# Kernel optimization log

Measured on AMD Instinct MI355X. Metric: run time of the kernel, lower is better.

Reference implementation:

```python
import jax, jax.numpy as jnp
import numpy as np
from jax import lax

KS = 3
N = KS * KS  # 9 sampling locations per output pixel


def conv2d(x, w, b, pad, dil=1):
    out = lax.conv_general_dilated(
        x, w, window_strides=(1, 1), padding=((pad, pad), (pad, pad)),
        rhs_dilation=(dil, dil), dimension_numbers=('NCHW', 'OIHW', 'NCHW'))
    return out + b[None, :, None, None]


def deform_conv(x, p_w, p_b, dw, db):
    # Pure deform-conv-v2 semantics: offsets from p_conv, bilinear gather on
    # zero-padded input, then 3x3 contraction over the 9 gathered samples.
    B, C, H, W = x.shape
    offset = conv2d(x, p_w, p_b, 1)                       # (B, 2N, H, W)
    xp = jnp.pad(x, ((0, 0), (0, 0), (1, 1), (1, 1)))     # zero pad by 1
    Hp, Wp = H + 2, W + 2
    rr = jnp.arange(-(KS // 2), KS // 2 + 1)
    pi, pj = jnp.meshgrid(rr, rr, indexing='ij')
    p_n = jnp.concatenate([pi.reshape(-1), pj.reshape(-1)]).astype(x.dtype)   # (2N,)
    gi, gj = jnp.meshgrid(jnp.arange(1, H + 1), jnp.arange(1, W + 1), indexing='ij')
    p0 = jnp.concatenate([jnp.broadcast_to(gi, (N, H, W)),
                          jnp.broadcast_to(gj, (N, H, W))], 0).astype(x.dtype)  # (2N,H,W)
    p = p0[None] + p_n[None, :, None, None] + offset      # (B, 2N, H, W)
    p = jnp.transpose(p, (0, 2, 3, 1))                    # (B, H, W, 2N)
    py, px = p[..., :N], p[..., N:]
    fy, fx = jnp.floor(py), jnp.floor(px)
    lt_y = jnp.clip(fy, 0, Hp - 1); lt_x = jnp.clip(fx, 0, Wp - 1)
    rb_y = jnp.clip(fy + 1, 0, Hp - 1); rb_x = jnp.clip(fx + 1, 0, Wp - 1)
    pyc = jnp.clip(py, 0, Hp - 1); pxc = jnp.clip(px, 0, Wp - 1)
    g_lt = (1 + (lt_y - pyc)) * (1 + (lt_x - pxc))
    g_rb = (1 - (rb_y - pyc)) * (1 - (rb_x - pxc))
    g_lb = (1 + (lt_y - pyc)) * (1 - (rb_x - pxc))
    g_rt = (1 - (rb_y - pyc)) * (1 + (lt_x - pxc))
    xf = xp.reshape(B, C, Hp * Wp)

    def gather(qy, qx):
        idx = (qy.astype(jnp.int32) * Wp + qx.astype(jnp.int32)).reshape(B, -1)
        g = jax.vmap(lambda xb, ib: jnp.take(xb, ib, axis=1))(xf, idx)
        return g.reshape(B, C, H, W, N)

    x_lt = gather(lt_y, lt_x); x_rb = gather(rb_y, rb_x)
    x_lb = gather(lt_y, rb_x); x_rt = gather(rb_y, lt_x)
    samples = (g_lt[:, None] * x_lt + g_rb[:, None] * x_rb
               + g_lb[:, None] * x_lb + g_rt[:, None] * x_rt)  # (B,C,H,W,N)
    out = jnp.einsum('bchwn,ocn->bohw', samples, dw.reshape(dw.shape[0], C, N))
    return out + db[None, :, None, None]


def reference(x, w1, b1, w2, b2, w3, b3, w4, b4, p_w, p_b, dw, db, cw, cb):
    branches = [(w1, b1, 1, 1.0), (w2, b2, 3, 3.0), (w3, b3, 5, 5.0), (w4, b4, 7, 7.0)]
    feats = [deform_conv(conv2d(x, w, b, d, d) * s, p_w, p_b, dw, db)
             for (w, b, d, s) in branches]
    combined = jnp.concatenate(feats, axis=1)             # (B, 4*Cout, H, W)
    return jax.nn.relu(conv2d(combined, cw, cb, 0))


def setup_inputs() -> dict:
    B, Cin, Cout, H, W = 4, 128, 64, 128, 128
    key = jax.random.key(0)
    ks = jax.random.split(key, 16)
    sc3 = 1.0 / np.sqrt(Cin * 9)      # fan-in scale for 3x3 convs
    sc1 = 1.0 / np.sqrt(4 * Cout)     # fan-in scale for 1x1 fuse conv
    scd = 1.0 / np.sqrt(Cout * 9)     # deform main conv
    inp = {'x': jax.random.normal(ks[0], (B, Cin, H, W), jnp.float32)}
    for i in range(4):
        inp[f'w{i+1}'] = jax.random.normal(ks[1 + i], (Cout, Cin, 3, 3), jnp.float32) * sc3
        inp[f'b{i+1}'] = jax.random.normal(ks[5 + i], (Cout,), jnp.float32) * 0.01
    inp['p_w'] = jax.random.normal(ks[9], (2 * N, Cout, 3, 3), jnp.float32) * 0.01
    inp['p_b'] = jax.random.normal(ks[10], (2 * N,), jnp.float32) * 0.01
    inp['dw'] = jax.random.normal(ks[11], (Cout, Cout, 3, 3), jnp.float32) * scd
    inp['db'] = jax.random.normal(ks[12], (Cout,), jnp.float32) * 0.01
    inp['cw'] = jax.random.normal(ks[13], (Cout, 4 * Cout, 1, 1), jnp.float32) * sc1
    inp['cb'] = jax.random.normal(ks[14], (Cout,), jnp.float32) * 0.01
    return inp
```

## Files before the change

### kernel.cpp

```cpp
#include <hip/hip_runtime.h>
#include <hip/hip_fp16.h>

#define H 128
#define W 128
#define CIN 128
#define COUT 64
#define HW (H*W)
#define XW 130
#define FSL (XW*XW*64)
#define XTD 144

typedef __half f16;
typedef __attribute__((ext_vector_type(8)))  _Float16 h16x8;
typedef __attribute__((ext_vector_type(16))) float f32x16;

__device__ __forceinline__ float b2f(f16 v){ return __half2float(v); }
__device__ __forceinline__ f16  f2b(float v){ return __float2half_rn(v); }
__device__ __forceinline__ unsigned pack2(float a, float b){
    unsigned short ua = __builtin_bit_cast(unsigned short, f2b(a));
    unsigned short ub = __builtin_bit_cast(unsigned short, f2b(b));
    return (unsigned)ua | ((unsigned)ub << 16);
}
__device__ __forceinline__ unsigned short b16u(float v){
    return __builtin_bit_cast(unsigned short, f2b(v));
}
__device__ __forceinline__ __half2 uh2(unsigned u){
    return __builtin_bit_cast(__half2, u);
}
__device__ __forceinline__ unsigned h2u(__half2 v){
    return __builtin_bit_cast(unsigned, v);
}
__device__ __forceinline__ unsigned bcasth2(float v){
    __half h = __float2half_rn(v);
    return h2u(__halves2half2(h, h));
}
__device__ __forceinline__ void gld16(const void* g, void* l){
    __builtin_amdgcn_global_load_lds(
        (const __attribute__((address_space(1))) void*)g,
        (__attribute__((address_space(3))) void*)l, 16, 0, 0);
}

__global__ __launch_bounds__(256) void k_prep(
    const float* __restrict__ w1, const float* __restrict__ w2,
    const float* __restrict__ w3, const float* __restrict__ w4,
    const float* __restrict__ dw, const float* __restrict__ cw,
    const float* __restrict__ pw,
    uint4* __restrict__ xt4, unsigned* __restrict__ wbt,
    unsigned* __restrict__ dwb2, unsigned* __restrict__ cwb2,
    unsigned* __restrict__ pwb)
{
    int bid = blockIdx.x;
    int t = threadIdx.x;
    if (bid < 1024){
        const int n4 = (4*XTD*XTD*64)/4;
        for (int i = bid*256 + t; i < n4; i += 1024*256)
            xt4[i] = make_uint4(0,0,0,0);
    } else if (bid < 1600){
        int tid = (bid-1024)*256 + t;
        int cpl = tid & 7;
        int oc  = (tid >> 3) & 63;
        int tap = (tid >> 9) % 9;
        int cg  = (tid / 4608) & 7;
        int d   = tid / 36864;
        const float* wt = (d==0)?w1:(d==1)?w2:(d==2)?w3:w4;
        int c = cg*8 + cpl;
        wbt[tid] = pack2(wt[((size_t)oc*CIN + 2*c  )*9 + tap],
                         wt[((size_t)oc*CIN + 2*c+1)*9 + tap]);
    } else if (bid < 1672){
        int i = (bid-1600)*256 + t;
        int n = i>>11, oc = (i>>5)&63, cp = i&31;
        dwb2[i] = pack2(dw[((size_t)oc*64 + 2*cp  )*9 + n],
                        dw[((size_t)oc*64 + 2*cp+1)*9 + n]);
    } else if (bid < 1704){
        int i = (bid-1672)*256 + t;
        int oc = i>>7, cp = i&127;
        cwb2[i] = pack2(cw[(size_t)oc*256 + 2*cp], cw[(size_t)oc*256 + 2*cp+1]);
    } else {
        int i = (bid-1704)*256 + t;
        int cl = i & 3, oc = (i>>2)&31, hf = (i>>7)&1, cq = (i>>8)&3, tap = i>>10;
        int c = cq*16 + hf*8 + cl*2;
        unsigned v = 0u;
        if (oc < 18)
            v = pack2(pw[((size_t)oc*64 + c  )*9 + tap],
                      pw[((size_t)oc*64 + c+1)*9 + tap]);
        pwb[i] = v;
    }
}

__global__ __launch_bounds__(256) void k_xprep(
    const float* __restrict__ x, unsigned* __restrict__ xt)
{
    int y = blockIdx.x, b = blockIdx.y;
    int t = threadIdx.x;
    __shared__ float xsm[64*131];
    for (int ci0 = 0; ci0 < 128; ci0 += 64){
        for (int i=0;i<32;i++){
            int idx = t + 256*i;
            int col = idx & 127, ci = idx >> 7;
            xsm[ci*131 + col] = x[(((size_t)b*CIN + ci0+ci)*H + y)*W + col];
        }
        __syncthreads();
        for (int i=0;i<16;i++){
            int idx = t + 256*i;
            int cpg = idx & 31, col = idx >> 5;
            int cgg = (ci0 >> 4) + (cpg >> 3);
            int cpl = cpg & 7;
            unsigned u = pack2(xsm[(2*cpg)*131 + col], xsm[(2*cpg+1)*131 + col]);
            xt[((((size_t)b*8 + cgg)*XTD + y+8)*XTD + col+8)*8 + cpl] = u;
        }
        __syncthreads();
    }
}

__global__ __launch_bounds__(256,3) void k_branch_mfma(
    const unsigned* __restrict__ xt, const unsigned* __restrict__ wbt,
    const float* __restrict__ b1, const float* __restrict__ b2,
    const float* __restrict__ b3, const float* __restrict__ b4,
    f16* __restrict__ feats2)
{
    int bid = blockIdx.x;
    int xcd = bid & 7;
    int j   = bid >> 3;
    int zb  = xcd + 8*(j & 1);
    int hp  = j >> 1;
    int d = zb >> 2, b = zb & 3;
    int dil = 2*d + 1;
    int h0 = hp*2;
    const float* bs = (d==0)?b1:(d==1)?b2:(d==2)?b3:b4;
    const float scale = (float)dil;

    __shared__ unsigned smem[6912 + 4608];
    unsigned* As = smem;
    unsigned* Bs = smem + 6912;
    const unsigned short* As16 = (const unsigned short*)As;
    const unsigned short* Bs16 = (const unsigned short*)Bs;

    int t = threadIdx.x;
    int lane = t & 63;
    int w = t >> 6;
    int l31 = lane & 31;
    int half = lane >> 5;

    f16* fb = feats2 + (size_t)zb*FSL;
    if (t < 32){
        int yy = h0 + 1 + (t>>4);
        int side = (t>>3)&1;
        int q = t & 7;
        uint4 z = make_uint4(0,0,0,0);
        *(uint4*)((unsigned short*)fb + ((size_t)yy*XW + side*129)*64 + q*8) = z;
    }
    if (hp == 0){
        uint4 z = make_uint4(0,0,0,0);
        for (int i=t; i<2080; i+=256){
            int row = i / 1040;
            int r = i % 1040;
            int xx = r >> 3, q = r & 7;
            *(uint4*)((unsigned short*)fb + ((size_t)(row*129)*XW + xx)*64 + q*8) = z;
        }
    }

    f32x16 acc[2][2];
    #pragma unroll
    for (int i=0;i<2;i++)
      #pragma unroll
      for (int jj=0;jj<2;jj++)
        #pragma unroll
        for (int e=0;e<16;e++) acc[i][jj][e] = 0.f;

    const unsigned* xtb_b = xt + (size_t)b*8*XTD*XTD*8;
    int r = w >> 1;
    int pxb = (w & 1) * 64;

    for (int cg=0; cg<8; cg++){
        const unsigned* xs_cg = xtb_b + (size_t)cg*XTD*XTD*8;
        #pragma unroll
        for (int i=0;i<7;i++){
            int idx4 = t + 256*i;
            if (idx4 < 1728){
                int row6 = idx4 / 288;
                int rem  = idx4 - row6*288;
                int hf   = rem / 144;
                int s    = rem - hf*144;
                int ky = row6 >> 1, rr = row6 & 1;
                int yy = h0 + rr + (ky-1)*dil + 8;
                gld16(xs_cg + ((size_t)yy*XTD + (s + 8 - dil))*8 + hf*4,
                      &As[idx4*4]);
            }
        }
        const unsigned* wb_cg = wbt + ((size_t)d*8 + cg)*4608;
        #pragma unroll
        for (int i=0;i<5;i++){
            int idx4 = t + 256*i;
            if (idx4 < 1152){
                int tap = idx4 >> 7;
                int hf  = (idx4 >> 6) & 1;
                int oc  = idx4 & 63;
                gld16(wb_cg + ((size_t)tap*64 + oc)*8 + hf*4,
                      &Bs[idx4*4]);
            }
        }
        __syncthreads();
        #pragma unroll
        for (int tap=0; tap<9; tap++){
            int ky = tap/3, kx = tap%3;
            int arow = ((ky*2 + r)*2 + half)*144;
            int brow = (tap*2 + half)*64;
            h16x8 a0  = *(const h16x8*)(As16 + (arow + pxb      + l31 + kx*dil)*8);
            h16x8 a1  = *(const h16x8*)(As16 + (arow + pxb + 32 + l31 + kx*dil)*8);
            h16x8 bb0 = *(const h16x8*)(Bs16 + (brow      + l31)*8);
            h16x8 bb1 = *(const h16x8*)(Bs16 + (brow + 32 + l31)*8);
            acc[0][0] = __builtin_amdgcn_mfma_f32_32x32x16_f16(a0, bb0, acc[0][0], 0,0,0);
            acc[0][1] = __builtin_amdgcn_mfma_f32_32x32x16_f16(a0, bb1, acc[0][1], 0,0,0);
            acc[1][0] = __builtin_amdgcn_mfma_f32_32x32x16_f16(a1, bb0, acc[1][0], 0,0,0);
            acc[1][1] = __builtin_amdgcn_mfma_f32_32x32x16_f16(a1, bb1, acc[1][1], 0,0,0);
        }
        __syncthreads();
    }

    unsigned short* ep = (unsigned short*)smem;
    float bias0 = bs[l31], bias1 = bs[32 + l31];
    #pragma unroll
    for (int i=0;i<2;i++){
      #pragma unroll
      for (int jj=0;jj<2;jj++){
        int oc = jj*32 + l31;
        float bj = jj ? bias1 : bias0;
        #pragma unroll
        for (int rg=0; rg<4; rg++){
            int m0 = 64*w + 32*i + 8*rg + 4*half;
            #pragma unroll
            for (int e=0;e<4;e++)
                ep[(m0+e)*64 + oc] = b16u((acc[i][jj][4*rg+e] + bj)*scale);
        }
      }
    }
    __syncthreads();
    {
        int row = t >> 7, pxm = t & 127;
        unsigned short* drow = (unsigned short*)fb + ((size_t)(h0+1+row)*XW + pxm + 1)*64;
        const unsigned short* srow = ep + t*64;
        #pragma unroll
        for (int q=0;q<8;q++)
            *(uint4*)(drow + q*8) = *(const uint4*)(srow + q*8);
    }
}

__global__ __launch_bounds__(256,2) void k_offset_mfma(
    const f16* __restrict__ feats2,
    const unsigned* __restrict__ pwb,
    const float* __restrict__ pb,
    f16* __restrict__ offs)
{
    int bid = blockIdx.x;
    int xcd  = bid & 7;
    int h    = (bid >> 3) & 127;
    int pass = bid >> 10;
    int zb   = xcd + 8*pass;

    int t = threadIdx.x;
    int lane = t & 63, w = t >> 6;
    int l31 = lane & 31, half = lane >> 5;

    __shared__ unsigned short xs[3*132*68];

    const unsigned short* fin = (const unsigned short*)(feats2 + (size_t)zb*FSL);
    for (int i=t; i<3120; i+=256){
        int row = i / 1040;
        int r   = i % 1040;
        int col = r >> 3, q = r & 7;
        uint4 v = *(const uint4*)(fin + ((size_t)(h+row)*XW + col)*64 + q*8);
        *(uint4*)&xs[(row*132 + col)*68 + q*8] = v;
    }
    __syncthreads();

    f32x16 acc;
    #pragma unroll
    for (int e=0;e<16;e++) acc[e] = 0.f;

    int pxw = 32*w + l31;
    #pragma unroll
    for (int tap=0; tap<9; tap++){
        int ky = tap/3, kx = tap%3;
        const unsigned short* arow = &xs[(ky*132 + pxw + kx)*68 + half*8];
        const unsigned* brow = pwb + (((size_t)tap*4)*2 + half)*128 + l31*4;
        #pragma unroll
        for (int cq=0; cq<4; cq++){
            h16x8 a  = *(const h16x8*)(arow + cq*16);
            h16x8 b0 = *(const h16x8*)(brow + cq*256);
            acc = __builtin_amdgcn_mfma_f32_32x32x16_f16(a, b0, acc, 0,0,0);
        }
    }
    __syncthreads();

    unsigned short* ep = (unsigned short*)xs;
    if (l31 < 18){
        float bias = pb[l31];
        #pragma unroll
        for (int rg=0; rg<4; rg++){
            int m0 = 32*w + 4*half + 8*rg;
            #pragma unroll
            for (int e=0;e<4;e++)
                ep[l31*132 + m0+e] = b16u(acc[4*rg+e] + bias);
        }
    }
    __syncthreads();
    unsigned short* obase = (unsigned short*)(offs + (size_t)zb*18*HW) ;
    for (int i=t; i<288; i+=256){
        int oc = i >> 4, sg = i & 15;
        *(uint4*)(obase + (size_t)oc*HW + h*W + sg*8) = *(const uint4*)(ep + oc*132 + sg*8);
    }
}

__global__ __launch_bounds__(256,4) void k_deform_mfma(
    const f16* __restrict__ feats2,
    const f16* __restrict__ offs,
    const unsigned* __restrict__ dwb2,
    const float* __restrict__ db,
    f16* __restrict__ dout2)
{
    int bid = blockIdx.x;
    int xcd  = bid & 7;
    int h    = (bid >> 3) & 127;
    int pass = bid >> 10;
    int zb   = xcd + 8*pass;

    int t = threadIdx.x;
    int lane = t & 63, w = t >> 6;
    int l31 = lane & 31, half = lane >> 5;
    int pxg = t >> 3;
    int cq  = t & 7;
    int sub_w = cq >> 1;
    int hf8   = cq & 1;

    #define AROW 516
    __shared__ unsigned smem_d[8*AROW + 2304 + 1024];
    unsigned* Asu = smem_d;
    unsigned* Bsu = smem_d + 8*AROW;
    unsigned* Cd  = smem_d + 8*AROW + 2304;

    const f16* obase = offs + (size_t)zb*18*HW + h*W;
    const unsigned short* fbase = (const unsigned short*)(feats2 + (size_t)zb*FSL);

    f32x16 acc0, acc1;
    #pragma unroll
    for (int e=0;e<16;e++){ acc0[e]=0.f; acc1[e]=0.f; }

    for (int n=0; n<9; n++){
        const uint4* dsrc = (const uint4*)(dwb2 + n*2048);
        #pragma unroll
        for (int i=0;i<2;i++){
            int j = t + 256*i;
            int idx4 = j*4;
            int oc = idx4 >> 5, cp = idx4 & 31;
            *(uint4*)&Bsu[oc*36 + cp] = dsrc[j];
        }
        if (t < 128){
            float offy = b2f(obase[n*HW + t]);
            float offx = b2f(obase[(n+9)*HW + t]);
            float py  = (float)(h + n/3) + offy;
            float pxf = (float)(t + n%3) + offx;
            float fy = floorf(py), fx = floorf(pxf);
            float lty = fminf(fmaxf(fy,     0.f),129.f);
            float ltx = fminf(fmaxf(fx,     0.f),129.f);
            float rby = fminf(fmaxf(fy+1.f, 0.f),129.f);
            float rbx = fminf(fmaxf(fx+1.f, 0.f),129.f);
            float pyc = fminf(fmaxf(py,     0.f),129.f);
            float pxc = fminf(fmaxf(pxf,    0.f),129.f);
            float ay = 1.f + (lty-pyc), by = 1.f - (rby-pyc);
            float ax = 1.f + (ltx-pxc), bx = 1.f - (rbx-pxc);
            unsigned* cp = &Cd[t*8];
            cp[0] = bcasth2(ay*ax);
            cp[1] = bcasth2(ay*bx);
            cp[2] = bcasth2(by*ax);
            cp[3] = bcasth2(by*bx);
            cp[4] = (unsigned)(((int)lty*XW + (int)ltx)*64);
            cp[5] = (unsigned)(((int)rbx - (int)ltx)*64);
            cp[6] = (unsigned)(((int)rby - (int)lty)*XW*64);
        }
        __syncthreads();
        #pragma unroll
        for (int s=0; s<4; s++){
            int px = s*32 + pxg;
            const unsigned* cp = &Cd[px*8];
            uint4 c0 = *(const uint4*)cp;
            uint4 c1 = *(const uint4*)(cp + 4);
            __half2 wlt = uh2(c0.x);
            __half2 wlb = uh2(c0.y);
            __half2 wrt = uh2(c0.z);
            __half2 wrb = uh2(c0.w);
            int base = (int)c1.x;
            int dxo  = (int)c1.y;
            int dyo  = (int)c1.z;

            const unsigned short* fc = fbase + base + cq*8;
            unsigned LT[4], LB[4], RT[4], RB[4];
            *(uint4*)LT = *(const uint4*)(fc);
            *(uint4*)LB = *(const uint4*)(fc+dxo);
            *(uint4*)RT = *(const uint4*)(fc+dyo);
            *(uint4*)RB = *(const uint4*)(fc+dyo+dxo);
            unsigned pk[4];
            #pragma unroll
            for (int jq=0;jq<4;jq++){
                __half2 r = __hmul2(wlt, uh2(LT[jq]));
                r = __hfma2(wlb, uh2(LB[jq]), r);
                r = __hfma2(wrt, uh2(RT[jq]), r);
                r = __hfma2(wrb, uh2(RB[jq]), r);
                pk[jq] = h2u(r);
            }
            uint4 av; av.x=pk[0]; av.y=pk[1]; av.z=pk[2]; av.w=pk[3];
            *(uint4*)&Asu[(sub_w*2 + hf8)*AROW + px*4] = av;
        }
        __syncthreads();
        const unsigned short* As16 = (const unsigned short*)Asu;
        const unsigned short* Bs16 = (const unsigned short*)Bsu;
        #pragma unroll
        for (int s=0;s<4;s++){
            h16x8 a  = *(const h16x8*)(As16 + (s*2+half)*(AROW*2) + (32*w + l31)*8);
            h16x8 b0 = *(const h16x8*)(Bs16 + (l31*36 + s*8 + half*4)*2);
            h16x8 b1 = *(const h16x8*)(Bs16 + ((32+l31)*36 + s*8 + half*4)*2);
            acc0 = __builtin_amdgcn_mfma_f32_32x32x16_f16(a, b0, acc0, 0,0,0);
            acc1 = __builtin_amdgcn_mfma_f32_32x32x16_f16(a, b1, acc1, 0,0,0);
        }
        __syncthreads();
    }

    unsigned short* ep = (unsigned short*)smem_d;
    #pragma unroll
    for (int nt=0; nt<2; nt++){
        int oc = nt*32 + l31;
        float bias = db[oc];
        const f32x16& A = nt ? acc1 : acc0;
        #pragma unroll
        for (int rg=0; rg<4; rg++){
            int m0 = 32*w + 4*half + 8*rg;
            #pragma unroll
            for (int e=0;e<4;e++)
                ep[(m0+e)*64 + oc] = b16u(A[4*rg+e] + bias);
        }
    }
    __syncthreads();
    uint4* dst = (uint4*)((unsigned short*)dout2 + ((size_t)zb*128 + h)*(128*64));
    #pragma unroll
    for (int i=0;i<4;i++)
        dst[t + 256*i] = ((const uint4*)ep)[t + 256*i];
    #undef AROW
}

__global__ __launch_bounds__(256,2) void k_combine_mfma(
    const f16* __restrict__ dout2,
    const unsigned* __restrict__ cwb2,
    const float* __restrict__ cb,
    float* __restrict__ out)
{
    int h = blockIdx.x, b = blockIdx.y;
    int t = threadIdx.x;
    int px = t & 127, hf = t >> 7;
    int lane = t & 63, w = t >> 6, l31 = lane & 31, half = lane >> 5;

    __shared__ unsigned Bsu[64*132];
    __shared__ unsigned Asu2[1024];

    for (int i=t; i<8192; i+=256){
        int oc = i>>7, cp = i&127;
        Bsu[oc*132 + cp] = cwb2[i];
    }
    f32x16 acc0, acc1;
    #pragma unroll
    for (int e=0;e<16;e++){ acc0[e]=0.f; acc1[e]=0.f; }

    const unsigned short* dbase0 = (const unsigned short*)dout2;
    size_t rowsel = ((size_t)b*128 + h)*128 + px;
    uint4 v = *(const uint4*)(dbase0 + rowsel*64 + hf*8);
    for (int kc=0; kc<16; kc++){
        *(uint4*)&Asu2[(hf*128+px)*4] = v;
        __syncthreads();
        if (kc < 15){
            int kn = kc+1;
            int d = kn>>2, c16 = kn&3;
            v = *(const uint4*)(dbase0 + ((size_t)d*4*128*128*64 + rowsel*64) + c16*16 + hf*8);
        }
        const unsigned short* As16 = (const unsigned short*)Asu2;
        const unsigned short* Bs16 = (const unsigned short*)Bsu;
        h16x8 a  = *(const h16x8*)(As16 + (half*128 + 32*w + l31)*8);
        h16x8 b0 = *(const h16x8*)(Bs16 + (l31*132 + kc*8 + half*4)*2);
        h16x8 b1 = *(const h16x8*)(Bs16 + ((32+l31)*132 + kc*8 + half*4)*2);
        acc0 = __builtin_amdgcn_mfma_f32_32x32x16_f16(a, b0, acc0, 0,0,0);
        acc1 = __builtin_amdgcn_mfma_f32_32x32x16_f16(a, b1, acc1, 0,0,0);
        __syncthreads();
    }
    float* ep = (float*)Bsu;
    #pragma unroll
    for (int nt=0; nt<2; nt++){
        int oc = nt*32 + l31;
        float bias = cb[oc];
        const f32x16& A = nt ? acc1 : acc0;
        #pragma unroll
        for (int rg=0; rg<4; rg++){
            int m0 = 32*w + 4*half + 8*rg;
            #pragma unroll
            for (int e=0;e<4;e++)
                ep[oc*132 + m0+e] = fmaxf(A[4*rg+e] + bias, 0.f);
        }
    }
    __syncthreads();
    for (int i=t; i<2048; i+=256){
        int oc = i>>5, sg = i&31;
        *(uint4*)&out[(((size_t)b*64+oc)*128 + h)*128 + sg*4] = *(const uint4*)&ep[oc*132 + sg*4];
    }
}

extern "C" void kernel_launch(void* const* d_in, const int* in_sizes, int n_in,
                              void* d_out, int out_size, void* d_ws, size_t ws_size,
                              hipStream_t stream) {
    const float* x  = (const float*)d_in[0];
    const float* w1 = (const float*)d_in[1];
    const float* b1 = (const float*)d_in[2];
    const float* w2 = (const float*)d_in[3];
    const float* b2 = (const float*)d_in[4];
    const float* w3 = (const float*)d_in[5];
    const float* b3 = (const float*)d_in[6];
    const float* w4 = (const float*)d_in[7];
    const float* b4 = (const float*)d_in[8];
    const float* pw = (const float*)d_in[9];
    const float* pb = (const float*)d_in[10];
    const float* dw = (const float*)d_in[11];
    const float* db = (const float*)d_in[12];
    const float* cw = (const float*)d_in[13];
    const float* cb = (const float*)d_in[14];
    float* out = (float*)d_out;

    f16* feats2 = (f16*)d_ws;
    f16* offs   = feats2 + (size_t)16*FSL;
    f16* region2 = offs + (size_t)16*18*HW;
    f16* dout2  = region2;
    unsigned* xt  = (unsigned*)region2;
    unsigned* wbt = xt + (size_t)4*8*XTD*XTD*8;
    unsigned* dwb2 = (unsigned*)(dout2 + (size_t)16*128*128*64);
    unsigned* cwb2 = dwb2 + 18432;
    unsigned* pwb  = cwb2 + 8192;

    k_prep        <<<dim3(1740),    256, 0, stream>>>(w1,w2,w3,w4, dw, cw, pw,
                                                      (uint4*)xt, wbt, dwb2, cwb2, pwb);
    k_xprep       <<<dim3(128,4),   256, 0, stream>>>(x, xt);
    k_branch_mfma <<<dim3(1024),    256, 0, stream>>>(xt, wbt, b1,b2,b3,b4, feats2);
    k_offset_mfma <<<dim3(2048),    256, 0, stream>>>(feats2, pwb, pb, offs);
    k_deform_mfma <<<dim3(2048),    256, 0, stream>>>(feats2, offs, dwb2, db, dout2);
    k_combine_mfma<<<dim3(128,4),   256, 0, stream>>>(dout2, cwb2, cb, out);
}
```

Before: 299.0 us.

## Prefetch deform coords, read MFMA B-fragments from global, drop combine LDS staging

```diff
diff --git a/kernel.cpp b/kernel.cpp
--- a/kernel.cpp
+++ b/kernel.cpp
@@ -68,12 +68,21 @@
                          wt[((size_t)oc*CIN + 2*c+1)*9 + tap]);
     } else if (bid < 1672){
         int i = (bid-1600)*256 + t;
-        int n = i>>11, oc = (i>>5)&63, cp = i&31;
+        int n = i>>11;
+        int s = (i>>9)&3;
+        int hf = (i>>8)&1;
+        int oc = (i>>2)&63;
+        int cl = i&3;
+        int cp = s*8 + hf*4 + cl;
         dwb2[i] = pack2(dw[((size_t)oc*64 + 2*cp  )*9 + n],
                         dw[((size_t)oc*64 + 2*cp+1)*9 + n]);
     } else if (bid < 1704){
         int i = (bid-1672)*256 + t;
-        int oc = i>>7, cp = i&127;
+        int kc = i>>9;
+        int hf = (i>>8)&1;
+        int oc = (i>>2)&63;
+        int cl = i&3;
+        int cp = kc*8 + hf*4 + cl;
         cwb2[i] = pack2(cw[(size_t)oc*256 + 2*cp], cw[(size_t)oc*256 + 2*cp+1]);
     } else {
         int i = (bid-1704)*256 + t;
@@ -311,6 +320,31 @@
     }
 }
 
+__device__ __forceinline__ void coords_px(
+    const f16* __restrict__ obase, int h, int n, int px, unsigned* cp)
+{
+    float offy = b2f(obase[n*HW + px]);
+    float offx = b2f(obase[(n+9)*HW + px]);
+    float py  = (float)(h + n/3) + offy;
+    float pxf = (float)(px + n%3) + offx;
+    float fy = floorf(py), fx = floorf(pxf);
+    float lty = fminf(fmaxf(fy,     0.f),129.f);
+    float ltx = fminf(fmaxf(fx,     0.f),129.f);
+    float rby = fminf(fmaxf(fy+1.f, 0.f),129.f);
+    float rbx = fminf(fmaxf(fx+1.f, 0.f),129.f);
+    float pyc = fminf(fmaxf(py,     0.f),129.f);
+    float pxc = fminf(fmaxf(pxf,    0.f),129.f);
+    float ay = 1.f + (lty-pyc), by = 1.f - (rby-pyc);
+    float ax = 1.f + (ltx-pxc), bx = 1.f - (rbx-pxc);
+    cp[0] = bcasth2(ay*ax);
+    cp[1] = bcasth2(ay*bx);
+    cp[2] = bcasth2(by*ax);
+    cp[3] = bcasth2(by*bx);
+    cp[4] = (unsigned)(((int)lty*XW + (int)ltx)*64);
+    cp[5] = (unsigned)(((int)rbx - (int)ltx)*64);
+    cp[6] = (unsigned)(((int)rby - (int)lty)*XW*64);
+}
+
 __global__ __launch_bounds__(256,4) void k_deform_mfma(
     const f16* __restrict__ feats2,
     const f16* __restrict__ offs,
@@ -333,10 +367,9 @@
     int hf8   = cq & 1;
 
     #define AROW 516
-    __shared__ unsigned smem_d[8*AROW + 2304 + 1024];
+    __shared__ unsigned smem_d[8*AROW + 2048];
     unsigned* Asu = smem_d;
-    unsigned* Bsu = smem_d + 8*AROW;
-    unsigned* Cd  = smem_d + 8*AROW + 2304;
+    unsigned* Cd  = smem_d + 8*AROW;
 
     const f16* obase = offs + (size_t)zb*18*HW + h*W;
     const unsigned short* fbase = (const unsigned short*)(feats2 + (size_t)zb*FSL);
@@ -345,79 +378,56 @@
     #pragma unroll
     for (int e=0;e<16;e++){ acc0[e]=0.f; acc1[e]=0.f; }
 
+    if (t < 128) coords_px(obase, h, 0, t, Cd + t*8);
+    __syncthreads();
+
     for (int n=0; n<9; n++){
-        const uint4* dsrc = (const uint4*)(dwb2 + n*2048);
-        #pragma unroll
-        for (int i=0;i<2;i++){
-            int j = t + 256*i;
-            int idx4 = j*4;
-            int oc = idx4 >> 5, cp = idx4 & 31;
-            *(uint4*)&Bsu[oc*36 + cp] = dsrc[j];
-        }
-        if (t < 128){
-            float offy = b2f(obase[n*HW + t]);
-            float offx = b2f(obase[(n+9)*HW + t]);
-            float py  = (float)(h + n/3) + offy;
-            float pxf = (float)(t + n%3) + offx;
-            float fy = floorf(py), fx = floorf(pxf);
-            float lty = fminf(fmaxf(fy,     0.f),129.f);
-            float ltx = fminf(fmaxf(fx,     0.f),129.f);
-            float rby = fminf(fmaxf(fy+1.f, 0.f),129.f);
-            float rbx = fminf(fmaxf(fx+1.f, 0.f),129.f);
-            float pyc = fminf(fmaxf(py,     0.f),129.f);
-            float pxc = fminf(fmaxf(pxf,    0.f),129.f);
-            float ay = 1.f + (lty-pyc), by = 1.f - (rby-pyc);
-            float ax = 1.f + (ltx-pxc), bx = 1.f - (rbx-pxc);
-            unsigned* cp = &Cd[t*8];
-            cp[0] = bcasth2(ay*ax);
-            cp[1] = bcasth2(ay*bx);
-            cp[2] = bcasth2(by*ax);
-            cp[3] = bcasth2(by*bx);
-            cp[4] = (unsigned)(((int)lty*XW + (int)ltx)*64);
-            cp[5] = (unsigned)(((int)rbx - (int)ltx)*64);
-            cp[6] = (unsigned)(((int)rby - (int)lty)*XW*64);
-        }
-        __syncthreads();
+        unsigned* Cdc = Cd + (n&1)*1024;
+        unsigned* Cdn = Cd + ((n+1)&1)*1024;
+
+        unsigned LT[16], LB[16], RT[16], RB[16];
+        #pragma unroll
+        for (int s=0; s<4; s++){
+            const unsigned* cp = Cdc + (s*32+pxg)*8;
+            uint4 c1 = *(const uint4*)(cp + 4);
+            int dxo = (int)c1.y, dyo = (int)c1.z;
+            const unsigned short* fc = fbase + (int)c1.x + cq*8;
+            *(uint4*)&LT[4*s] = *(const uint4*)(fc);
+            *(uint4*)&LB[4*s] = *(const uint4*)(fc+dxo);
+            *(uint4*)&RT[4*s] = *(const uint4*)(fc+dyo);
+            *(uint4*)&RB[4*s] = *(const uint4*)(fc+dyo+dxo);
+        }
+        if (n < 8 && t < 128) coords_px(obase, h, n+1, t, Cdn + t*8);
+
         #pragma unroll
         for (int s=0; s<4; s++){
             int px = s*32 + pxg;
-            const unsigned* cp = &Cd[px*8];
-            uint4 c0 = *(const uint4*)cp;
-            uint4 c1 = *(const uint4*)(cp + 4);
+            uint4 c0 = *(const uint4*)(Cdc + px*8);
             __half2 wlt = uh2(c0.x);
             __half2 wlb = uh2(c0.y);
             __half2 wrt = uh2(c0.z);
             __half2 wrb = uh2(c0.w);
-            int base = (int)c1.x;
-            int dxo  = (int)c1.y;
-            int dyo  = (int)c1.z;
-
-            const unsigned short* fc = fbase + base + cq*8;
-            unsigned LT[4], LB[4], RT[4], RB[4];
-            *(uint4*)LT = *(const uint4*)(fc);
-            *(uint4*)LB = *(const uint4*)(fc+dxo);
-            *(uint4*)RT = *(const uint4*)(fc+dyo);
-            *(uint4*)RB = *(const uint4*)(fc+dyo+dxo);
             unsigned pk[4];
             #pragma unroll
             for (int jq=0;jq<4;jq++){
-                __half2 r = __hmul2(wlt, uh2(LT[jq]));
-                r = __hfma2(wlb, uh2(LB[jq]), r);
-                r = __hfma2(wrt, uh2(RT[jq]), r);
-                r = __hfma2(wrb, uh2(RB[jq]), r);
+                __half2 r = __hmul2(wlt, uh2(LT[4*s+jq]));
+                r = __hfma2(wlb, uh2(LB[4*s+jq]), r);
+                r = __hfma2(wrt, uh2(RT[4*s+jq]), r);
+                r = __hfma2(wrb, uh2(RB[4*s+jq]), r);
                 pk[jq] = h2u(r);
             }
             uint4 av; av.x=pk[0]; av.y=pk[1]; av.z=pk[2]; av.w=pk[3];
             *(uint4*)&Asu[(sub_w*2 + hf8)*AROW + px*4] = av;
         }
         __syncthreads();
+
         const unsigned short* As16 = (const unsigned short*)Asu;
-        const unsigned short* Bs16 = (const unsigned short*)Bsu;
+        const unsigned short* dnb16 = (const unsigned short*)(dwb2 + n*2048);
         #pragma unroll
         for (int s=0;s<4;s++){
             h16x8 a  = *(const h16x8*)(As16 + (s*2+half)*(AROW*2) + (32*w + l31)*8);
-            h16x8 b0 = *(const h16x8*)(Bs16 + (l31*36 + s*8 + half*4)*2);
-            h16x8 b1 = *(const h16x8*)(Bs16 + ((32+l31)*36 + s*8 + half*4)*2);
+            h16x8 b0 = *(const h16x8*)(dnb16 + ((s*2+half)*64 + l31)*8);
+            h16x8 b1 = *(const h16x8*)(dnb16 + ((s*2+half)*64 + 32+l31)*8);
             acc0 = __builtin_amdgcn_mfma_f32_32x32x16_f16(a, b0, acc0, 0,0,0);
             acc1 = __builtin_amdgcn_mfma_f32_32x32x16_f16(a, b1, acc1, 0,0,0);
         }
@@ -454,41 +464,33 @@
 {
     int h = blockIdx.x, b = blockIdx.y;
     int t = threadIdx.x;
-    int px = t & 127, hf = t >> 7;
     int lane = t & 63, w = t >> 6, l31 = lane & 31, half = lane >> 5;
 
-    __shared__ unsigned Bsu[64*132];
-    __shared__ unsigned Asu2[1024];
-
-    for (int i=t; i<8192; i+=256){
-        int oc = i>>7, cp = i&127;
-        Bsu[oc*132 + cp] = cwb2[i];
-    }
+    __shared__ float ep2[64*132];
+
     f32x16 acc0, acc1;
     #pragma unroll
     for (int e=0;e<16;e++){ acc0[e]=0.f; acc1[e]=0.f; }
 
     const unsigned short* dbase0 = (const unsigned short*)dout2;
-    size_t rowsel = ((size_t)b*128 + h)*128 + px;
-    uint4 v = *(const uint4*)(dbase0 + rowsel*64 + hf*8);
+    const unsigned short* cb16 = (const unsigned short*)cwb2;
+    size_t rowsel2 = ((size_t)b*128 + h)*128 + (32*w + l31);
+
+    unsigned AV[64];
+    #pragma unroll
     for (int kc=0; kc<16; kc++){
-        *(uint4*)&Asu2[(hf*128+px)*4] = v;
-        __syncthreads();
-        if (kc < 15){
-            int kn = kc+1;
-            int d = kn>>2, c16 = kn&3;
-            v = *(const uint4*)(dbase0 + ((size_t)d*4*128*128*64 + rowsel*64) + c16*16 + hf*8);
-        }
-        const unsigned short* As16 = (const unsigned short*)Asu2;
-        const unsigned short* Bs16 = (const unsigned short*)Bsu;
-        h16x8 a  = *(const h16x8*)(As16 + (half*128 + 32*w + l31)*8);
-        h16x8 b0 = *(const h16x8*)(Bs16 + (l31*132 + kc*8 + half*4)*2);
-        h16x8 b1 = *(const h16x8*)(Bs16 + ((32+l31)*132 + kc*8 + half*4)*2);
+        *(uint4*)&AV[kc*4] = *(const uint4*)(
+            dbase0 + (size_t)(kc>>2)*(4*HW*64) + rowsel2*64 + (kc&3)*16 + half*8);
+    }
+    #pragma unroll
+    for (int kc=0; kc<16; kc++){
+        h16x8 a  = __builtin_bit_cast(h16x8, *(uint4*)&AV[kc*4]);
+        h16x8 b0 = *(const h16x8*)(cb16 + ((kc*2+half)*64 + l31)*8);
+        h16x8 b1 = *(const h16x8*)(cb16 + ((kc*2+half)*64 + 32+l31)*8);
         acc0 = __builtin_amdgcn_mfma_f32_32x32x16_f16(a, b0, acc0, 0,0,0);
         acc1 = __builtin_amdgcn_mfma_f32_32x32x16_f16(a, b1, acc1, 0,0,0);
-        __syncthreads();
-    }
-    float* ep = (float*)Bsu;
+    }
+
     #pragma unroll
     for (int nt=0; nt<2; nt++){
         int oc = nt*32 + l31;
@@ -499,13 +501,13 @@
             int m0 = 32*w + 4*half + 8*rg;
             #pragma unroll
             for (int e=0;e<4;e++)
-                ep[oc*132 + m0+e] = fmaxf(A[4*rg+e] + bias, 0.f);
+                ep2[oc*132 + m0+e] = fmaxf(A[4*rg+e] + bias, 0.f);
         }
     }
     __syncthreads();
     for (int i=t; i<2048; i+=256){
         int oc = i>>5, sg = i&31;
-        *(uint4*)&out[(((size_t)b*64+oc)*128 + h)*128 + sg*4] = *(const uint4*)&ep[oc*132 + sg*4];
+        *(uint4*)&out[(((size_t)b*64+oc)*128 + h)*128 + sg*4] = *(const uint4*)&ep2[oc*132 + sg*4];
     }
 }
 
```

After: 309.5 us. 1.04x slower.
